# Optimization experiments

Hardware: AMD Instinct MI355X
Metric: run time of the kernel (lower is better)

The kernel has to match this reference:

```python
import jax, jax.numpy as jnp
import numpy as np
import math

BS, SEQ, HID = 1, 2048, 2048
NH, NKV, HD = 32, 8, 64
BASE = 10000.0


def rotate_half(x):
    x1, x2 = x[..., : x.shape[-1] // 2], x[..., x.shape[-1] // 2 :]
    return jnp.concatenate((-x2, x1), axis=-1)


def setup_inputs() -> dict:
    key = jax.random.key(0)
    ks = jax.random.split(key, 6)
    s = 0.02
    return {
        "x": jax.random.normal(ks[0], (BS, SEQ, HID), dtype=jnp.float32),
        "attention_mask": jnp.zeros((BS, SEQ), dtype=jnp.float32),
        "position_ids": jnp.broadcast_to(jnp.arange(SEQ, dtype=jnp.int64 if jax.config.jax_enable_x64 else jnp.int32), (BS, SEQ)),
        "wq": jax.random.normal(ks[1], (HID, NH * HD), dtype=jnp.float32) * s,
        "wk": jax.random.normal(ks[2], (HID, NKV * HD), dtype=jnp.float32) * s,
        "wv": jax.random.normal(ks[3], (HID, NKV * HD), dtype=jnp.float32) * s,
        "wo": jax.random.normal(ks[4], (NH * HD, HID), dtype=jnp.float32) * s,
    }


def reference(x, attention_mask, position_ids, wq, wk, wv, wo):
    bs, seq, _ = x.shape
    groups = NH // NKV

    q = (x @ wq).reshape(bs, seq, NH, HD).transpose(0, 2, 1, 3)   # [b,H,S,D]
    k = (x @ wk).reshape(bs, seq, NKV, HD).transpose(0, 2, 1, 3)  # [b,Hkv,S,D]
    v = (x @ wv).reshape(bs, seq, NKV, HD).transpose(0, 2, 1, 3)

    # rotary embedding
    inv_freq = 1.0 / (BASE ** (jnp.arange(0, HD, 2, dtype=jnp.float32) / HD))  # [D/2]
    freqs = position_ids.astype(jnp.float32)[:, :, None] * inv_freq[None, None, :]  # [b,S,D/2]
    emb = jnp.concatenate((freqs, freqs), axis=-1)               # [b,S,D]
    cos = jnp.cos(emb)[:, None, :, :].astype(x.dtype)            # [b,1,S,D]
    sin = jnp.sin(emb)[:, None, :, :].astype(x.dtype)
    q = q * cos + rotate_half(q) * sin
    k = k * cos + rotate_half(k) * sin

    # repeat_kv (GQA expand)
    k = jnp.repeat(k, groups, axis=1)  # [b,H,S,D]
    v = jnp.repeat(v, groups, axis=1)

    scores = jnp.einsum("bhqd,bhkd->bhqk", q, k) / math.sqrt(HD)
    scores = scores + attention_mask[:, None, None, :]
    attn = jax.nn.softmax(scores.astype(jnp.float32), axis=-1).astype(q.dtype)
    out = jnp.einsum("bhqk,bhkd->bhqd", attn, v)                 # [b,H,S,D]
    out = out.transpose(0, 2, 1, 3).reshape(bs, seq, NH * HD)
    return out @ wo
```

## Files before the change

kernel.cpp:

```cpp
#include <hip/hip_runtime.h>

#define SEQ 2048
#define HID 2048
#define NH  32
#define NKV 8
#define HD  64

typedef _Float16 f16;
typedef __attribute__((ext_vector_type(4))) _Float16 f16x4;
typedef __attribute__((ext_vector_type(8))) _Float16 f16x8;
typedef __attribute__((ext_vector_type(4))) float    f32x4;

__device__ __forceinline__ f32x4 mfma_16x16x32(f16x8 a, f16x8 b, f32x4 c) {
    return __builtin_amdgcn_mfma_f32_16x16x32_f16(a, b, c, 0, 0, 0);
}

__device__ __forceinline__ void async16(const void* g, void* l) {
    __builtin_amdgcn_global_load_lds(
        (const __attribute__((address_space(1))) void*)g,
        (__attribute__((address_space(3))) void*)l,
        16, 0, 0);
}

__global__ void prep_all(const float* __restrict__ x,
                         const float* __restrict__ wq, const float* __restrict__ wk,
                         const float* __restrict__ wv, const float* __restrict__ wo,
                         f16* __restrict__ xb,
                         f16* __restrict__ Wcat, f16* __restrict__ woT) {
    __shared__ float tile[32][33];
    int z = blockIdx.z;
    int tx = threadIdx.x, ty = threadIdx.y;
    if (z == 4) {
        int idx = (blockIdx.y * 64 + blockIdx.x) * 256 + ty * 32 + tx;
        int i = idx * 4;
        float4 v = *(const float4*)(x + i);
        f16x4 o = { (f16)v.x, (f16)v.y, (f16)v.z, (f16)v.w };
        *(f16x4*)(xb + i) = o;
        return;
    }
    const float* src; f16* dst; int C;
    if      (z == 0) { src = wq; dst = Wcat;                         C = 2048; }
    else if (z == 1) { src = wk; dst = Wcat + (size_t)2048 * 2048;   C = 512;  }
    else if (z == 2) { src = wv; dst = Wcat + (size_t)2560 * 2048;   C = 512;  }
    else             { src = wo; dst = woT;                          C = 2048; }
    int c0 = blockIdx.x * 32, r0 = blockIdx.y * 32;
    if (c0 >= C) return;
#pragma unroll
    for (int i = 0; i < 32; i += 8)
        tile[ty + i][tx] = src[(size_t)(r0 + ty + i) * C + c0 + tx];
    __syncthreads();
#pragma unroll
    for (int i = 0; i < 32; i += 8)
        dst[(size_t)(c0 + ty + i) * 2048 + r0 + tx] = (f16)tile[tx][ty + i];
}

template <int MODE>
__global__ __launch_bounds__(256)
void gemm_bt(const f16* __restrict__ A, const f16* __restrict__ BT,
             float* __restrict__ Cf, f16* __restrict__ Q, f16* __restrict__ Kk,
             f16* __restrict__ VT, const int* __restrict__ pos,
             const float* __restrict__ mask, int N, int K) {
    __shared__ f16 As[2][64 * 32];
    __shared__ f16 Bs[2][128 * 32];
    int t = threadIdx.x;
    int w = t >> 6, lane = t & 63, quad = lane >> 4, l15 = lane & 15;
    int wm = w >> 1, wn = w & 1;
    int m0 = blockIdx.y * 64, n0 = blockIdx.x * 128;

    int srow  = t >> 2;
    int skoff = (t & 3) * 8;
    const f16* Ag = A  + (size_t)(m0 + srow) * K + skoff;
    const f16* Bg = BT + (size_t)(n0 + srow) * K + skoff;

    f32x4 acc[2][4] = {};

    async16(Ag,                  &As[0][w * 512]);
    async16(Bg,                  &Bs[0][w * 512]);
    async16(Bg + (size_t)64 * K, &Bs[0][2048 + w * 512]);
    __syncthreads();

    int b = 0;
    for (int kt = 32; kt <= K; kt += 32) {
        if (kt < K) {
            async16(Ag + kt,                  &As[b ^ 1][w * 512]);
            async16(Bg + kt,                  &Bs[b ^ 1][w * 512]);
            async16(Bg + (size_t)64 * K + kt, &Bs[b ^ 1][2048 + w * 512]);
        }
        f16x8 af[2], bf[4];
#pragma unroll
        for (int mi = 0; mi < 2; mi++)
            af[mi] = *(const f16x8*)(&As[b][(wm * 32 + mi * 16 + l15) * 32 + quad * 8]);
#pragma unroll
        for (int ni = 0; ni < 4; ni++)
            bf[ni] = *(const f16x8*)(&Bs[b][(wn * 64 + ni * 16 + l15) * 32 + quad * 8]);
#pragma unroll
        for (int mi = 0; mi < 2; mi++)
#pragma unroll
            for (int ni = 0; ni < 4; ni++)
                acc[mi][ni] = mfma_16x16x32(af[mi], bf[ni], acc[mi][ni]);
        __syncthreads();
        b ^= 1;
    }

    int rb  = m0 + wm * 32 + quad * 4;
    int cbh = n0 + wn * 64;
    if (MODE == 0) {
        if (cbh < (NH + NKV) * HD) {
            bool isQ = cbh < NH * HD;
            f16* dst = isQ ? (Q  + (size_t)(cbh >> 6) * SEQ * HD)
                           : (Kk + (size_t)((cbh - NH * HD) >> 6) * SEQ * HD);
            float scale = isQ ? 0.18033688011112042f : 1.0f;
            float fr[2];
#pragma unroll
            for (int ni = 0; ni < 2; ni++)
                fr[ni] = __builtin_amdgcn_exp2f(
                    (float)(ni * 16 + l15) * -0.41524101186092029f);
#pragma unroll
            for (int mi = 0; mi < 2; mi++)
#pragma unroll
                for (int r = 0; r < 4; r++) {
                    int row = rb + mi * 16 + r;
                    float pv = (float)pos[row];
#pragma unroll
                    for (int ni = 0; ni < 2; ni++) {
                        float sn, cs;
                        __sincosf(pv * fr[ni], &sn, &cs);
                        float x1 = acc[mi][ni][r], x2 = acc[mi][ni + 2][r];
                        int d = ni * 16 + l15;
                        dst[(size_t)row * HD + d]      = (f16)(scale * (x1 * cs - x2 * sn));
                        dst[(size_t)row * HD + d + 32] = (f16)(scale * (x2 * cs + x1 * sn));
                    }
                }
        } else {
            const float LOG2E = 1.4426950408889634f;
#pragma unroll
            for (int mi = 0; mi < 2; mi++) {
                float4 mv = *(const float4*)(mask + rb + mi * 16);
                float em[4];
#pragma unroll
                for (int r = 0; r < 4; r++)
                    em[r] = __builtin_amdgcn_exp2f((&mv.x)[r] * LOG2E);
#pragma unroll
                for (int ni = 0; ni < 4; ni++) {
                    int c2 = cbh - (NH + NKV) * HD + ni * 16 + l15;
                    f16x4 v4 = { (f16)(acc[mi][ni][0] * em[0]),
                                 (f16)(acc[mi][ni][1] * em[1]),
                                 (f16)(acc[mi][ni][2] * em[2]),
                                 (f16)(acc[mi][ni][3] * em[3]) };
                    *(f16x4*)(VT + (size_t)c2 * SEQ + rb + mi * 16) = v4;
                }
            }
        }
    } else {
#pragma unroll
        for (int mi = 0; mi < 2; mi++)
#pragma unroll
            for (int ni = 0; ni < 4; ni++)
#pragma unroll
                for (int r = 0; r < 4; r++)
                    Cf[(size_t)(rb + mi * 16 + r) * N + cbh + ni * 16 + l15] =
                        acc[mi][ni][r];
    }
}

__global__ __launch_bounds__(256)
void attn_fused(const f16* __restrict__ Qb, const f16* __restrict__ Kb,
                const f16* __restrict__ VTb, const float* __restrict__ mask,
                f16* __restrict__ ctx) {
    __shared__ f16 Ks[2][64 * 64];
    __shared__ f16 Vs[2][64 * 64];
    __shared__ f16 Em[SEQ];

    int t = threadIdx.x, w = t >> 6, lane = t & 63, quad = lane >> 4, l15 = lane & 15;
    int h = blockIdx.y, kvh = h >> 2;
    int qbase = blockIdx.x * 128 + w * 32;
    const f16* Qh = Qb  + (size_t)h   * SEQ * HD;
    const f16* Kh = Kb  + (size_t)kvh * SEQ * HD;
    const f16* Vh = VTb + (size_t)kvh * HD * SEQ;
    int sw = l15 & 7;
    const float LOG2E = 1.4426950408889634f;

    {
        int idx = t * 8;
        float4 ma = *(const float4*)(mask + idx);
        float4 mb = *(const float4*)(mask + idx + 4);
        f16x8 e;
        e[0] = (f16)__builtin_amdgcn_exp2f(ma.x * LOG2E);
        e[1] = (f16)__builtin_amdgcn_exp2f(ma.y * LOG2E);
        e[2] = (f16)__builtin_amdgcn_exp2f(ma.z * LOG2E);
        e[3] = (f16)__builtin_amdgcn_exp2f(ma.w * LOG2E);
        e[4] = (f16)__builtin_amdgcn_exp2f(mb.x * LOG2E);
        e[5] = (f16)__builtin_amdgcn_exp2f(mb.y * LOG2E);
        e[6] = (f16)__builtin_amdgcn_exp2f(mb.z * LOG2E);
        e[7] = (f16)__builtin_amdgcn_exp2f(mb.w * LOG2E);
        *(f16x8*)(&Em[idx]) = e;
    }

    int r8 = lane >> 3;
    int cc = (lane & 7) ^ r8;
    int gk = 32 * (w >> 1) + 4 * (w & 1) + 8 * (r8 >> 2) + (r8 & 3);
    const f16* kg0 = Kh + (size_t)gk * HD + cc * 8;
    const f16* kg1 = kg0 + (size_t)16 * HD;
    const f16* vg0 = Vh + (size_t)(w * 16 + r8) * SEQ + cc * 8;
    const f16* vg1 = vg0 + 8 * SEQ;
    int lr0 = (w * 16) * 64, lr1 = (w * 16 + 8) * 64;

    async16(kg0, &Ks[0][lr0]);
    async16(kg1, &Ks[0][lr1]);
    async16(vg0, &Vs[0][lr0]);
    async16(vg1, &Vs[0][lr1]);

    f16x8 bq[2][2];
#pragma unroll
    for (int qg = 0; qg < 2; qg++)
#pragma unroll
        for (int ks = 0; ks < 2; ks++)
            bq[qg][ks] = *(const f16x8*)(Qh + (size_t)(qbase + qg * 16 + l15) * HD
                                            + ks * 32 + quad * 8);

    f32x4 o[4][2] = {};
    f32x4 ol[2]   = {};

    __syncthreads();
    int b = 0;

    for (int ktl = 0; ktl < SEQ / 64; ktl++) {
        if (ktl + 1 < SEQ / 64) {
            kg0 += 64 * HD; kg1 += 64 * HD; vg0 += 64; vg1 += 64;
            async16(kg0, &Ks[b ^ 1][lr0]);
            async16(kg1, &Ks[b ^ 1][lr1]);
            async16(vg0, &Vs[b ^ 1][lr0]);
            async16(vg1, &Vs[b ^ 1][lr1]);
        }
        const f16* Kb_ = &Ks[b][0];
        const f16* Vb_ = &Vs[b][0];

        f32x4 st[4][2] = {};
#pragma unroll
        for (int ni = 0; ni < 4; ni++) {
            const f16* kr = Kb_ + (ni * 16 + l15) * 64;
            f16x8 ak0 = *(const f16x8*)(kr + (quad ^ sw) * 8);
            f16x8 ak1 = *(const f16x8*)(kr + ((4 | quad) ^ sw) * 8);
#pragma unroll
            for (int qg = 0; qg < 2; qg++) {
                st[ni][qg] = mfma_16x16x32(ak0, bq[qg][0], st[ni][qg]);
                st[ni][qg] = mfma_16x16x32(ak1, bq[qg][1], st[ni][qg]);
            }
        }
        f16x8 pb[2][2];
#pragma unroll
        for (int ni = 0; ni < 4; ni++)
#pragma unroll
            for (int qg = 0; qg < 2; qg++)
#pragma unroll
                for (int r = 0; r < 4; r++)
                    pb[qg][ni >> 1][(ni & 1) * 4 + r] =
                        (f16)__builtin_amdgcn_exp2f(st[ni][qg][r]);
        f16x8 em0 = *(const f16x8*)(&Em[ktl * 64 + quad * 8]);
        f16x8 em1 = *(const f16x8*)(&Em[ktl * 64 + 32 + quad * 8]);
#pragma unroll
        for (int qg = 0; qg < 2; qg++) {
            ol[qg] = mfma_16x16x32(em0, pb[qg][0], ol[qg]);
            ol[qg] = mfma_16x16x32(em1, pb[qg][1], ol[qg]);
        }
#pragma unroll
        for (int dt = 0; dt < 4; dt++) {
            const f16* vr = Vb_ + (dt * 16 + l15) * 64;
            f16x8 av0 = *(const f16x8*)(vr + (quad ^ sw) * 8);
            f16x8 av1 = *(const f16x8*)(vr + ((4 | quad) ^ sw) * 8);
#pragma unroll
            for (int qg = 0; qg < 2; qg++) {
                o[dt][qg] = mfma_16x16x32(av0, pb[qg][0], o[dt][qg]);
                o[dt][qg] = mfma_16x16x32(av1, pb[qg][1], o[dt][qg]);
            }
        }
        __syncthreads();
        b ^= 1;
    }

    float linv[2] = { 1.0f / ol[0][0], 1.0f / ol[1][0] };

#pragma unroll
    for (int dt = 0; dt < 4; dt++)
#pragma unroll
        for (int qg = 0; qg < 2; qg++) {
            f16x4 v4 = { (f16)(o[dt][qg][0] * linv[qg]),
                         (f16)(o[dt][qg][1] * linv[qg]),
                         (f16)(o[dt][qg][2] * linv[qg]),
                         (f16)(o[dt][qg][3] * linv[qg]) };
            *(f16x4*)(ctx + (size_t)(qbase + qg * 16 + l15) * (NH * HD)
                          + h * 64 + dt * 16 + quad * 4) = v4;
        }
}

extern "C" void kernel_launch(void* const* d_in, const int* in_sizes, int n_in,
                              void* d_out, int out_size, void* d_ws, size_t ws_size,
                              hipStream_t stream) {
    const float* x    = (const float*)d_in[0];
    const float* mask = (const float*)d_in[1];
    const int*   pos  = (const int*)  d_in[2];
    const float* wq   = (const float*)d_in[3];
    const float* wk   = (const float*)d_in[4];
    const float* wv   = (const float*)d_in[5];
    const float* wo   = (const float*)d_in[6];
    float* out = (float*)d_out;

    char* ws = (char*)d_ws;
    f16* xb   = (f16*)(ws);
    f16* ctx  = (f16*)(ws);
    f16* Wcat = (f16*)(ws + ((size_t)8  << 20));
    f16* woT  = (f16*)(ws + ((size_t)20 << 20));
    f16* Qb   = (f16*)(ws + ((size_t)28 << 20));
    f16* Kb   = (f16*)(ws + ((size_t)36 << 20));
    f16* VTb  = (f16*)(ws + ((size_t)38 << 20));

    prep_all<<<dim3(64, 64, 5), dim3(32, 8), 0, stream>>>(
        x, wq, wk, wv, wo, xb, Wcat, woT);

    gemm_bt<0><<<dim3(3072 / 128, 2048 / 64), 256, 0, stream>>>(
        xb, Wcat, nullptr, Qb, Kb, VTb, pos, mask, 3072, 2048);

    attn_fused<<<dim3(SEQ / 128, NH), 256, 0, stream>>>(
        Qb, Kb, VTb, mask, ctx);

    gemm_bt<1><<<dim3(2048 / 128, 2048 / 64), 256, 0, stream>>>(
        ctx, woT, out, nullptr, nullptr, nullptr, nullptr, nullptr, 2048, 2048);
}
```

Measured before the change: 233.4 us.

## Double GEMM K-tile with XOR-swizzled LDS and use packed f16 conversions

The GEMM K-tile grows from 32 to 64 and shared-memory staging is rearranged with an XOR swizzle, which halves the number of barriers and loop iterations and should reduce LDS bank conflicts. Separately, scalar f32-to-f16 conversions in the GEMM epilogue and the attention kernel are replaced with packed round-toward-zero conversions (cvt_pkrtz), and swizzle offsets are hoisted out of the attention loop. In exchange, LDS use doubles, which may lower occupancy, and rounding changes from nearest to toward-zero.

```diff
diff --git a/kernel.cpp b/kernel.cpp
--- a/kernel.cpp
+++ b/kernel.cpp
@@ -9,6 +9,7 @@
 typedef _Float16 f16;
 typedef __attribute__((ext_vector_type(4))) _Float16 f16x4;
 typedef __attribute__((ext_vector_type(8))) _Float16 f16x8;
+typedef __attribute__((ext_vector_type(2))) __fp16   h16x2;
 typedef __attribute__((ext_vector_type(4))) float    f32x4;
 
 __device__ __forceinline__ f32x4 mfma_16x16x32(f16x8 a, f16x8 b, f32x4 c) {
@@ -60,44 +61,60 @@
              float* __restrict__ Cf, f16* __restrict__ Q, f16* __restrict__ Kk,
              f16* __restrict__ VT, const int* __restrict__ pos,
              const float* __restrict__ mask, int N, int K) {
-    __shared__ f16 As[2][64 * 32];
-    __shared__ f16 Bs[2][128 * 32];
+    __shared__ f16 As[2][64 * 64];
+    __shared__ f16 Bs[2][128 * 64];
     int t = threadIdx.x;
     int w = t >> 6, lane = t & 63, quad = lane >> 4, l15 = lane & 15;
     int wm = w >> 1, wn = w & 1;
     int m0 = blockIdx.y * 64, n0 = blockIdx.x * 128;
-
-    int srow  = t >> 2;
-    int skoff = (t & 3) * 8;
-    const f16* Ag = A  + (size_t)(m0 + srow) * K + skoff;
-    const f16* Bg = BT + (size_t)(n0 + srow) * K + skoff;
+    int sw = l15 & 7;
+
+    int r8 = lane >> 3;
+    int cc = (lane & 7) ^ r8;
+    const f16* Ag0 = A  + (size_t)(m0 + w * 16 + r8) * K + cc * 8;
+    const f16* Ag1 = Ag0 + (size_t)8 * K;
+    const f16* Bg  = BT + (size_t)(n0 + w * 32 + r8) * K + cc * 8;
 
     f32x4 acc[2][4] = {};
 
-    async16(Ag,                  &As[0][w * 512]);
-    async16(Bg,                  &Bs[0][w * 512]);
-    async16(Bg + (size_t)64 * K, &Bs[0][2048 + w * 512]);
+    async16(Ag0, &As[0][w * 1024]);
+    async16(Ag1, &As[0][w * 1024 + 512]);
+#pragma unroll
+    for (int g = 0; g < 4; g++)
+        async16(Bg + (size_t)(8 * g) * K, &Bs[0][w * 2048 + g * 512]);
     __syncthreads();
 
     int b = 0;
-    for (int kt = 32; kt <= K; kt += 32) {
+    for (int kt = 64; kt <= K; kt += 64) {
         if (kt < K) {
-            async16(Ag + kt,                  &As[b ^ 1][w * 512]);
-            async16(Bg + kt,                  &Bs[b ^ 1][w * 512]);
-            async16(Bg + (size_t)64 * K + kt, &Bs[b ^ 1][2048 + w * 512]);
-        }
-        f16x8 af[2], bf[4];
+            async16(Ag0 + kt, &As[b ^ 1][w * 1024]);
+            async16(Ag1 + kt, &As[b ^ 1][w * 1024 + 512]);
+#pragma unroll
+            for (int g = 0; g < 4; g++)
+                async16(Bg + (size_t)(8 * g) * K + kt, &Bs[b ^ 1][w * 2048 + g * 512]);
+        }
+        f16x8 af[2][2], bf[4][2];
+#pragma unroll
+        for (int mi = 0; mi < 2; mi++) {
+            int row = wm * 32 + mi * 16 + l15;
+#pragma unroll
+            for (int kh = 0; kh < 2; kh++)
+                af[mi][kh] = *(const f16x8*)(&As[b][row * 64 + ((kh * 4 + quad) ^ sw) * 8]);
+        }
+#pragma unroll
+        for (int ni = 0; ni < 4; ni++) {
+            int row = wn * 64 + ni * 16 + l15;
+#pragma unroll
+            for (int kh = 0; kh < 2; kh++)
+                bf[ni][kh] = *(const f16x8*)(&Bs[b][row * 64 + ((kh * 4 + quad) ^ sw) * 8]);
+        }
 #pragma unroll
         for (int mi = 0; mi < 2; mi++)
-            af[mi] = *(const f16x8*)(&As[b][(wm * 32 + mi * 16 + l15) * 32 + quad * 8]);
-#pragma unroll
-        for (int ni = 0; ni < 4; ni++)
-            bf[ni] = *(const f16x8*)(&Bs[b][(wn * 64 + ni * 16 + l15) * 32 + quad * 8]);
-#pragma unroll
-        for (int mi = 0; mi < 2; mi++)
-#pragma unroll
-            for (int ni = 0; ni < 4; ni++)
-                acc[mi][ni] = mfma_16x16x32(af[mi], bf[ni], acc[mi][ni]);
+#pragma unroll
+            for (int ni = 0; ni < 4; ni++) {
+                acc[mi][ni] = mfma_16x16x32(af[mi][0], bf[ni][0], acc[mi][ni]);
+                acc[mi][ni] = mfma_16x16x32(af[mi][1], bf[ni][1], acc[mi][ni]);
+            }
         __syncthreads();
         b ^= 1;
     }
@@ -143,10 +160,11 @@
 #pragma unroll
                 for (int ni = 0; ni < 4; ni++) {
                     int c2 = cbh - (NH + NKV) * HD + ni * 16 + l15;
-                    f16x4 v4 = { (f16)(acc[mi][ni][0] * em[0]),
-                                 (f16)(acc[mi][ni][1] * em[1]),
-                                 (f16)(acc[mi][ni][2] * em[2]),
-                                 (f16)(acc[mi][ni][3] * em[3]) };
+                    f16x4 v4;
+                    ((h16x2*)&v4)[0] = __builtin_amdgcn_cvt_pkrtz(
+                        acc[mi][ni][0] * em[0], acc[mi][ni][1] * em[1]);
+                    ((h16x2*)&v4)[1] = __builtin_amdgcn_cvt_pkrtz(
+                        acc[mi][ni][2] * em[2], acc[mi][ni][3] * em[3]);
                     *(f16x4*)(VT + (size_t)c2 * SEQ + rb + mi * 16) = v4;
                 }
             }
@@ -185,14 +203,14 @@
         float4 ma = *(const float4*)(mask + idx);
         float4 mb = *(const float4*)(mask + idx + 4);
         f16x8 e;
-        e[0] = (f16)__builtin_amdgcn_exp2f(ma.x * LOG2E);
-        e[1] = (f16)__builtin_amdgcn_exp2f(ma.y * LOG2E);
-        e[2] = (f16)__builtin_amdgcn_exp2f(ma.z * LOG2E);
-        e[3] = (f16)__builtin_amdgcn_exp2f(ma.w * LOG2E);
-        e[4] = (f16)__builtin_amdgcn_exp2f(mb.x * LOG2E);
-        e[5] = (f16)__builtin_amdgcn_exp2f(mb.y * LOG2E);
-        e[6] = (f16)__builtin_amdgcn_exp2f(mb.z * LOG2E);
-        e[7] = (f16)__builtin_amdgcn_exp2f(mb.w * LOG2E);
+        ((h16x2*)&e)[0] = __builtin_amdgcn_cvt_pkrtz(
+            __builtin_amdgcn_exp2f(ma.x * LOG2E), __builtin_amdgcn_exp2f(ma.y * LOG2E));
+        ((h16x2*)&e)[1] = __builtin_amdgcn_cvt_pkrtz(
+            __builtin_amdgcn_exp2f(ma.z * LOG2E), __builtin_amdgcn_exp2f(ma.w * LOG2E));
+        ((h16x2*)&e)[2] = __builtin_amdgcn_cvt_pkrtz(
+            __builtin_amdgcn_exp2f(mb.x * LOG2E), __builtin_amdgcn_exp2f(mb.y * LOG2E));
+        ((h16x2*)&e)[3] = __builtin_amdgcn_cvt_pkrtz(
+            __builtin_amdgcn_exp2f(mb.z * LOG2E), __builtin_amdgcn_exp2f(mb.w * LOG2E));
         *(f16x8*)(&Em[idx]) = e;
     }
 
@@ -221,6 +239,8 @@
     f32x4 o[4][2] = {};
     f32x4 ol[2]   = {};
 
+    int c0 = (quad ^ sw) * 8, c1 = ((4 | quad) ^ sw) * 8;
+
     __syncthreads();
     int b = 0;
 
@@ -239,8 +259,8 @@
 #pragma unroll
         for (int ni = 0; ni < 4; ni++) {
             const f16* kr = Kb_ + (ni * 16 + l15) * 64;
-            f16x8 ak0 = *(const f16x8*)(kr + (quad ^ sw) * 8);
-            f16x8 ak1 = *(const f16x8*)(kr + ((4 | quad) ^ sw) * 8);
+            f16x8 ak0 = *(const f16x8*)(kr + c0);
+            f16x8 ak1 = *(const f16x8*)(kr + c1);
 #pragma unroll
             for (int qg = 0; qg < 2; qg++) {
                 st[ni][qg] = mfma_16x16x32(ak0, bq[qg][0], st[ni][qg]);
@@ -251,11 +271,16 @@
 #pragma unroll
         for (int ni = 0; ni < 4; ni++)
 #pragma unroll
-            for (int qg = 0; qg < 2; qg++)
-#pragma unroll
-                for (int r = 0; r < 4; r++)
-                    pb[qg][ni >> 1][(ni & 1) * 4 + r] =
-                        (f16)__builtin_amdgcn_exp2f(st[ni][qg][r]);
+            for (int qg = 0; qg < 2; qg++) {
+                h16x2 lo = __builtin_amdgcn_cvt_pkrtz(
+                    __builtin_amdgcn_exp2f(st[ni][qg][0]),
+                    __builtin_amdgcn_exp2f(st[ni][qg][1]));
+                h16x2 hi = __builtin_amdgcn_cvt_pkrtz(
+                    __builtin_amdgcn_exp2f(st[ni][qg][2]),
+                    __builtin_amdgcn_exp2f(st[ni][qg][3]));
+                ((h16x2*)&pb[qg][ni >> 1])[(ni & 1) * 2]     = lo;
+                ((h16x2*)&pb[qg][ni >> 1])[(ni & 1) * 2 + 1] = hi;
+            }
         f16x8 em0 = *(const f16x8*)(&Em[ktl * 64 + quad * 8]);
         f16x8 em1 = *(const f16x8*)(&Em[ktl * 64 + 32 + quad * 8]);
 #pragma unroll
@@ -266,8 +291,8 @@
 #pragma unroll
         for (int dt = 0; dt < 4; dt++) {
             const f16* vr = Vb_ + (dt * 16 + l15) * 64;
-            f16x8 av0 = *(const f16x8*)(vr + (quad ^ sw) * 8);
-            f16x8 av1 = *(const f16x8*)(vr + ((4 | quad) ^ sw) * 8);
+            f16x8 av0 = *(const f16x8*)(vr + c0);
+            f16x8 av1 = *(const f16x8*)(vr + c1);
 #pragma unroll
             for (int qg = 0; qg < 2; qg++) {
                 o[dt][qg] = mfma_16x16x32(av0, pb[qg][0], o[dt][qg]);
@@ -284,10 +309,11 @@
     for (int dt = 0; dt < 4; dt++)
 #pragma unroll
         for (int qg = 0; qg < 2; qg++) {
-            f16x4 v4 = { (f16)(o[dt][qg][0] * linv[qg]),
-                         (f16)(o[dt][qg][1] * linv[qg]),
-                         (f16)(o[dt][qg][2] * linv[qg]),
-                         (f16)(o[dt][qg][3] * linv[qg]) };
+            f16x4 v4;
+            ((h16x2*)&v4)[0] = __builtin_amdgcn_cvt_pkrtz(
+                o[dt][qg][0] * linv[qg], o[dt][qg][1] * linv[qg]);
+            ((h16x2*)&v4)[1] = __builtin_amdgcn_cvt_pkrtz(
+                o[dt][qg][2] * linv[qg], o[dt][qg][3] * linv[qg]);
             *(f16x4*)(ctx + (size_t)(qbase + qg * 16 + l15) * (NH * HD)
                           + h * 64 + dt * 16 + quad * 4) = v4;
         }
```

After: 220.4 us. 5.6% less time.
